# Kernel optimization log

Hardware: AMD Instinct MI355X
Metric: run time of the kernel (lower is better)

## Reference

```python
import jax, jax.numpy as jnp
import numpy as np

B, S, C, H = 2, 512, 25, 768


def setup_inputs() -> dict:
    key = jax.random.key(0)
    ks = jax.random.split(key, 10)
    sc = 1.0 / np.sqrt(H)
    return {
        "token_rep": jax.random.normal(ks[0], (B, S, H), jnp.float32),
        "label_rep": jax.random.normal(ks[1], (B, C, H), jnp.float32),
        # proj_token: Linear(H, 2H) stored as [in, out] for x @ W
        "Wt": jax.random.normal(ks[2], (H, 2 * H), jnp.float32) * sc,
        "bt": jnp.zeros((2 * H,), jnp.float32),
        # proj_label: Linear(H, 2H)
        "Wl": jax.random.normal(ks[3], (H, 2 * H), jnp.float32) * sc,
        "bl": jnp.zeros((2 * H,), jnp.float32),
        # out_mlp[0]: Linear(3H, 4H)
        "W1": jax.random.normal(ks[4], (3 * H, 4 * H), jnp.float32) * (1.0 / np.sqrt(3 * H)),
        "b1": jnp.zeros((4 * H,), jnp.float32),
        # out_mlp[3]: Linear(4H, 3)
        "W2": jax.random.normal(ks[5], (4 * H, 3), jnp.float32) * (1.0 / np.sqrt(4 * H)),
        "b2": jnp.zeros((3,), jnp.float32),
    }


def reference(token_rep, label_rep, Wt, bt, Wl, bl, W1, b1, W2, b2):
    h = token_rep.shape[-1]
    # project and split into (additive half, multiplicative half)
    tp = token_rep @ Wt + bt            # [B,S,2H]
    lp = label_rep @ Wl + bl            # [B,C,2H]
    ta, tb = tp[..., :h], tp[..., h:]
    la, lb = lp[..., :h], lp[..., h:]
    # First MLP layer on concat([ta, la, tb*lb]) without materializing the concat:
    # split W1 row-wise into the three input blocks.
    W1t, W1l, W1p = W1[:h], W1[h:2 * h], W1[2 * h:]
    hid = (ta @ W1t)[:, :, None, :] \
        + (la @ W1l)[:, None, :, :] \
        + jnp.einsum('bsh,bch,hf->bscf', tb, lb, W1p) \
        + b1                            # [B,S,C,4H]
    # Dropout is identity in eval mode.
    return jax.nn.relu(hid) @ W2 + b2   # [B,S,C,3]
```

## Files before the change

kernel.cpp:

```cpp
#include <hip/hip_runtime.h>
#include <hip/hip_bf16.h>
#include <cstdint>
#include <cstddef>

#define BB 2
#define SS 512
#define CC 25
#define HH 768
#define H2 1536
#define H3 2304
#define H4 3072
#define XC_STRIDE ((size_t)96 * 512 * 8)

typedef __attribute__((ext_vector_type(8))) short bf16x8;
typedef __attribute__((ext_vector_type(4))) float f32x4;

#define DEVINL static __device__ __forceinline__

DEVINL unsigned short f2bf(float f) {
  union { float f; unsigned u; } v; v.f = f;
  unsigned r = v.u + 0x7FFF + ((v.u >> 16) & 1);
  return (unsigned short)(r >> 16);
}
DEVINL float bf2f(unsigned short b) {
  union { unsigned u; float f; } v; v.u = ((unsigned)b) << 16; return v.f;
}

DEVINL void async16(const void* g, void* l) {
  __builtin_amdgcn_global_load_lds(
      (const __attribute__((address_space(1))) void*)g,
      (__attribute__((address_space(3))) void*)l, 16, 0, 0);
}

__global__ void k_prep(const float* __restrict__ token,
                       const float* __restrict__ label,
                       const float* __restrict__ b2,
                       const float* __restrict__ Wt,
                       const float* __restrict__ Wl,
                       const float* __restrict__ W1,
                       unsigned short* __restrict__ TC,
                       unsigned short* __restrict__ LC,
                       float* __restrict__ out,
                       unsigned short* __restrict__ WtC,
                       unsigned short* __restrict__ WlC,
                       unsigned short* __restrict__ W1C) {
  __shared__ float tile[64][33];
  const int bid = blockIdx.x;
  const int tid = threadIdx.x;
  if (bid < 408) {
    const float* in;
    unsigned short* o;
    int R, RP, kt, rt;
    if (bid < 384) {
      in = token; o = TC; R = 1024; RP = 1024; kt = bid % 24; rt = bid / 24;
    } else {
      in = label; o = LC; R = 50; RP = 64; kt = bid - 384; rt = 0;
    }
    const int k0 = kt * 32, r0 = rt * 64;
    const int tx = tid & 31, ty = tid >> 5;
#pragma unroll
    for (int i = 0; i < 8; i++) {
      int r = r0 + ty + i * 8;
      tile[ty + i * 8][tx] = in[(size_t)min(r, R - 1) * HH + k0 + tx];
    }
    __syncthreads();
    const int rl = tid & 63, kcl = tid >> 6;
    bf16x8 ov;
#pragma unroll
    for (int j = 0; j < 8; j++) ov[j] = (short)f2bf(tile[rl][kcl * 8 + j]);
    *(bf16x8*)&o[((size_t)((k0 >> 3) + kcl) * RP + r0 + rl) * 8] = ov;
  } else if (bid < 708) {
    int i = (bid - 408) * 256 + tid;
    if (i < BB * SS * CC * 3) out[i] = b2[i % 3];
  } else {
    const int wb = bid - 708;
    const float* in;
    unsigned short* o;
    int N, bx, by;
    if (wb < 3456) {
      in = W1; o = W1C; N = H4; bx = wb % 48; by = wb / 48;
    } else if (wb < 4032) {
      int b = wb - 3456; in = Wt; o = WtC; N = H2; bx = b % 24; by = b / 24;
    } else {
      int b = wb - 4032; in = Wl; o = WlC; N = H2; bx = b % 24; by = b / 24;
    }
    const int f = bx * 64 + (tid & 63);
    const int hc = by * 4 + (tid >> 6);
    bf16x8 ov;
#pragma unroll
    for (int j = 0; j < 8; j++)
      ov[j] = (short)f2bf(in[(size_t)(hc * 8 + j) * N + f]);
    *(bf16x8*)&o[((size_t)hc * N + f) * 8] = ov;
  }
}

DEVINL void mm_kloop(const unsigned short* __restrict__ Ab, int NRA, int MA,
                     int m0, const unsigned short* __restrict__ Bt, int NRB,
                     int n0, unsigned short* As, unsigned short* Bs,
                     f32x4 (&acc)[4][4]) {
  const int tid = threadIdx.x;
  const int lane = tid & 63;
  const int wave = tid >> 6;
  const int q = lane >> 4;
  const int li = lane & 15;
  const int wm = (wave >> 1) * 64;
  const int wn = (wave & 1) * 64;

  int sr[4], skc[4], sra[4];
#pragma unroll
  for (int j = 0; j < 4; j++) {
    int slot = j * 256 + tid;
    skc[j] = slot >> 7;
    sr[j] = slot & 127;
    sra[j] = min(m0 + sr[j], MA - 1);
  }
  auto stage = [&](int kciter) {
#pragma unroll
    for (int j = 0; j < 4; j++) {
      int slot = j * 256 + tid;
      async16(Ab + ((size_t)(kciter + skc[j]) * NRA + sra[j]) * 8,
              (char*)As + slot * 16);
      async16(Bt + ((size_t)(kciter + skc[j]) * NRB + n0 + sr[j]) * 8,
              (char*)Bs + slot * 16);
    }
  };

  stage(0);
  for (int it = 0; it < 12; it++) {
    __syncthreads();
#pragma unroll
    for (int ks = 0; ks < 2; ks++) {
      bf16x8 af[4], bb[4];
#pragma unroll
      for (int mi = 0; mi < 4; mi++)
        af[mi] = *(const bf16x8*)&As[((ks * 4 + q) * 128 + wm + mi * 16 + li) * 8];
#pragma unroll
      for (int ni = 0; ni < 4; ni++)
        bb[ni] = *(const bf16x8*)&Bs[((ks * 4 + q) * 128 + wn + ni * 16 + li) * 8];
#pragma unroll
      for (int mi = 0; mi < 4; mi++)
#pragma unroll
        for (int ni = 0; ni < 4; ni++)
          acc[mi][ni] = __builtin_amdgcn_mfma_f32_16x16x32_bf16(
              af[mi], bb[ni], acc[mi][ni], 0, 0, 0);
    }
    __syncthreads();
    if (it + 1 < 12) stage((it + 1) * 8);
  }
}

__global__ __launch_bounds__(256, 4) void k_mm1(
    const unsigned short* __restrict__ TC, const unsigned short* __restrict__ LC,
    const unsigned short* __restrict__ WtC, const unsigned short* __restrict__ WlC,
    const float* __restrict__ bt, const float* __restrict__ bl,
    unsigned short* __restrict__ TP, unsigned short* __restrict__ LP) {
  __shared__ __align__(16) unsigned short As[8 * 128 * 8];
  __shared__ __align__(16) unsigned short Bs[8 * 128 * 8];
  const int bid = blockIdx.x;
  const int nt = bid % 12, my = bid / 12;
  const bool tok = my < 8;
  const unsigned short* A = tok ? TC : LC;
  const unsigned short* Bt = tok ? WtC : WlC;
  const float* bias = tok ? bt : bl;
  unsigned short* C = tok ? TP : LP;
  const int NRA = tok ? 1024 : 64, MA = tok ? 1024 : 50;
  const int m0 = tok ? my * 128 : 0;
  const int ldc = NRA;
  const int n0 = nt * 128;

  f32x4 acc[4][4];
#pragma unroll
  for (int i = 0; i < 4; i++)
#pragma unroll
    for (int j = 0; j < 4; j++) acc[i][j] = (f32x4){0.f, 0.f, 0.f, 0.f};
  mm_kloop(A, NRA, MA, m0, Bt, H2, n0, As, Bs, acc);

  const int lane = threadIdx.x & 63, wave = threadIdx.x >> 6;
  const int q = lane >> 4, li = lane & 15;
  const int wm = (wave >> 1) * 64, wn = (wave & 1) * 64;
#pragma unroll
  for (int mi = 0; mi < 4; mi++)
#pragma unroll
    for (int rr = 0; rr < 4; rr++) {
      int row = m0 + wm + mi * 16 + q * 4 + rr;
      if (row < MA) {
#pragma unroll
        for (int ni = 0; ni < 4; ni++) {
          int col = n0 + wn + ni * 16 + li;
          C[((size_t)(col >> 3) * ldc + row) * 8 + (col & 7)] =
              f2bf(acc[mi][ni][rr] + bias[col]);
        }
      }
    }
}

__global__ __launch_bounds__(256, 4) void k_mm2(
    const unsigned short* __restrict__ TP, const unsigned short* __restrict__ LP,
    const unsigned short* __restrict__ W1C,
    float* __restrict__ base, float* __restrict__ al,
    unsigned short* __restrict__ XC) {
  __shared__ __align__(16) unsigned short As[8 * 128 * 8];
  __shared__ __align__(16) unsigned short Bs[8 * 128 * 8];
  const int bid = blockIdx.x;
  if (bid < 216) {
    const int nt = bid % 24, my = bid / 24;
    const bool tok = my < 8;
    const unsigned short* A = tok ? TP : LP;
    const unsigned short* Bt = tok ? W1C : W1C + (size_t)96 * H4 * 8;
    float* Cf = tok ? base : al;
    const int NRA = tok ? 1024 : 64, MA = tok ? 1024 : 50;
    const int m0 = tok ? my * 128 : 0;
    const int n0 = nt * 128;

    f32x4 acc[4][4];
#pragma unroll
    for (int i = 0; i < 4; i++)
#pragma unroll
      for (int j = 0; j < 4; j++) acc[i][j] = (f32x4){0.f, 0.f, 0.f, 0.f};
    mm_kloop(A, NRA, MA, m0, Bt, H4, n0, As, Bs, acc);

    const int lane = threadIdx.x & 63, wave = threadIdx.x >> 6;
    const int q = lane >> 4, li = lane & 15;
    const int wm = (wave >> 1) * 64, wn = (wave & 1) * 64;
#pragma unroll
    for (int mi = 0; mi < 4; mi++)
#pragma unroll
      for (int rr = 0; rr < 4; rr++) {
        int row = m0 + wm + mi * 16 + q * 4 + rr;
        if (row < MA) {
#pragma unroll
          for (int ni = 0; ni < 4; ni++) {
            int col = n0 + wn + ni * 16 + li;
            Cf[(size_t)row * H4 + col] = acc[mi][ni][rr];
          }
        }
      }
  } else {
    const int i = bid - 216;
    const int bc = i / 192;
    const int rem = i % 192;
    const int hc = rem >> 1;
    const int s = (rem & 1) * 256 + threadIdx.x;
    const int b = bc / CC;
    bf16x8 tv = *(const bf16x8*)&TP[((size_t)(96 + hc) * 1024 + b * 512 + s) * 8];
    bf16x8 lv = *(const bf16x8*)&LP[((size_t)(96 + hc) * 64 + bc) * 8];
    bf16x8 o;
#pragma unroll
    for (int j = 0; j < 8; j++)
      o[j] = (short)f2bf(bf2f((unsigned short)tv[j]) * bf2f((unsigned short)lv[j]));
    *(bf16x8*)&XC[(size_t)bc * XC_STRIDE + ((size_t)hc * 512 + s) * 8] = o;
  }
}

__global__ __launch_bounds__(256, 4) void k_scorer(
    const unsigned short* __restrict__ XC,
    const unsigned short* __restrict__ Bt,
    const float* __restrict__ base, const float* __restrict__ al,
    const float* __restrict__ b1, const float* __restrict__ W2,
    float* __restrict__ out) {
  __shared__ __align__(16) unsigned short As[8 * 128 * 8];
  __shared__ __align__(16) unsigned short Bs[8 * 128 * 8];
  const int tid = threadIdx.x;
  const int lane = tid & 63;
  const int wave = tid >> 6;
  const int q = lane >> 4;
  const int li = lane & 15;
  const int wm = (wave >> 1) * 64;
  const int wn = (wave & 1) * 64;

  const int n0 = blockIdx.x * 128;
  const int bc = blockIdx.y >> 2;
  const int m0 = (blockIdx.y & 3) * 128;
  const unsigned short* Ab = XC + (size_t)bc * XC_STRIDE;

  f32x4 acc[4][4];
#pragma unroll
  for (int i = 0; i < 4; i++)
#pragma unroll
    for (int j = 0; j < 4; j++) acc[i][j] = (f32x4){0.f, 0.f, 0.f, 0.f};
  mm_kloop(Ab, 512, 512, m0, Bt, H4, n0, As, Bs, acc);

  const int b = bc / CC, c = bc % CC;
  int fcol[4];
  float alb[4];
#pragma unroll
  for (int ni = 0; ni < 4; ni++) {
    int f = n0 + wn + ni * 16 + li;
    fcol[ni] = f;
    alb[ni] = al[(size_t)bc * H4 + f] + b1[f];
  }
  bf16x8 w2f[2];
#pragma unroll
  for (int ks = 0; ks < 2; ks++)
#pragma unroll
    for (int jj = 0; jj < 8; jj++) {
      int f = n0 + wn + ks * 32 + q * 8 + jj;
      float v = (li < 3) ? W2[(size_t)f * 3 + li] : 0.f;
      w2f[ks][jj] = (short)f2bf(v);
    }
  unsigned short* Ew = (unsigned short*)((char*)As + wave * 2304);

#pragma unroll
  for (int mi = 0; mi < 4; mi++) {
    float bs[4][4];
#pragma unroll
    for (int rr = 0; rr < 4; rr++) {
      int s_l = m0 + wm + mi * 16 + q * 4 + rr;
      const float* bp = base + (size_t)(b * SS + s_l) * H4;
#pragma unroll
      for (int ni = 0; ni < 4; ni++) bs[ni][rr] = bp[fcol[ni]];
    }
#pragma unroll
    for (int rr = 0; rr < 4; rr++)
#pragma unroll
      for (int ni = 0; ni < 4; ni++) {
        float v = acc[mi][ni][rr] + bs[ni][rr] + alb[ni];
        v = fmaxf(v, 0.f);
        Ew[(q * 4 + rr) * 72 + ni * 16 + li] = f2bf(v);
      }
    f32x4 oc = (f32x4){0.f, 0.f, 0.f, 0.f};
#pragma unroll
    for (int ks = 0; ks < 2; ks++) {
      bf16x8 ef = *(const bf16x8*)&Ew[li * 72 + ks * 32 + q * 8];
      oc = __builtin_amdgcn_mfma_f32_16x16x32_bf16(ef, w2f[ks], oc, 0, 0, 0);
    }
#pragma unroll
    for (int rr = 0; rr < 4; rr++) {
      int s_l = m0 + wm + mi * 16 + q * 4 + rr;
      if (li < 3)
        atomicAdd(&out[((size_t)(b * SS + s_l) * CC + c) * 3 + li], oc[rr]);
    }
  }
}


extern "C" void kernel_launch(void* const* d_in, const int* in_sizes, int n_in,
                              void* d_out, int out_size, void* d_ws, size_t ws_size,
                              hipStream_t stream) {
  (void)in_sizes; (void)n_in; (void)ws_size; (void)out_size;
  const float* token = (const float*)d_in[0];
  const float* label = (const float*)d_in[1];
  const float* Wt    = (const float*)d_in[2];
  const float* bt    = (const float*)d_in[3];
  const float* Wl    = (const float*)d_in[4];
  const float* bl    = (const float*)d_in[5];
  const float* W1    = (const float*)d_in[6];
  const float* b1    = (const float*)d_in[7];
  const float* W2    = (const float*)d_in[8];
  const float* b2    = (const float*)d_in[9];
  float* out = (float*)d_out;

  char* p = (char*)d_ws;
  auto alloc = [&](size_t bytes) {
    char* r = p;
    p += (bytes + 255) & ~(size_t)255;
    return r;
  };
  unsigned short* TC  = (unsigned short*)alloc((size_t)96 * 1024 * 8 * 2);
  unsigned short* LC  = (unsigned short*)alloc((size_t)96 * 64 * 8 * 2);
  unsigned short* WtC = (unsigned short*)alloc((size_t)96 * 1536 * 8 * 2);
  unsigned short* WlC = (unsigned short*)alloc((size_t)96 * 1536 * 8 * 2);
  unsigned short* W1C = (unsigned short*)alloc((size_t)288 * 3072 * 8 * 2);
  unsigned short* TP  = (unsigned short*)alloc((size_t)192 * 1024 * 8 * 2);
  unsigned short* LP  = (unsigned short*)alloc((size_t)192 * 64 * 8 * 2);
  unsigned short* XC  = (unsigned short*)alloc((size_t)CC * BB * XC_STRIDE * 2);
  float* base = (float*)alloc((size_t)BB * SS * H4 * 4);
  float* al   = (float*)alloc((size_t)BB * CC * H4 * 4);

  k_prep<<<5316, 256, 0, stream>>>(token, label, b2, Wt, Wl, W1,
                                   TC, LC, out, WtC, WlC, W1C);
  k_mm1<<<108, 256, 0, stream>>>(TC, LC, WtC, WlC, bt, bl, TP, LP);
  k_mm2<<<9816, 256, 0, stream>>>(TP, LP, W1C, base, al, XC);
  k_scorer<<<dim3(24, 200), 256, 0, stream>>>(
      XC, W1C + (size_t)192 * H4 * 8, base, al, b1, W2, out);
}
```

Before: 273.9 us.

## Double-buffer GEMM k-loop staging and store base/label partials in bf16

The shared GEMM k-loop moves from a single 8-chunk shared tile with two barriers per iteration to a two-buffer ping-pong of 4-chunk tiles with one barrier. The next tile's async loads are issued before the current tile's MFMAs, so global loads can overlap compute. Separately, the token and label partial products of the first MLP layer are stored as bf16, with b1 folded into the label part, instead of fp32. This halves their write and read traffic in the scorer epilogue, at the cost of an extra rounding step, and an added barrier protects reuse of shared memory in the epilogue.

```diff
diff --git a/kernel.cpp b/kernel.cpp
--- a/kernel.cpp
+++ b/kernel.cpp
@@ -106,46 +106,44 @@
   const int wm = (wave >> 1) * 64;
   const int wn = (wave & 1) * 64;
 
-  int sr[4], skc[4], sra[4];
-#pragma unroll
-  for (int j = 0; j < 4; j++) {
+  int sr[2], skc[2], sra[2];
+#pragma unroll
+  for (int j = 0; j < 2; j++) {
     int slot = j * 256 + tid;
     skc[j] = slot >> 7;
     sr[j] = slot & 127;
     sra[j] = min(m0 + sr[j], MA - 1);
   }
-  auto stage = [&](int kciter) {
-#pragma unroll
-    for (int j = 0; j < 4; j++) {
+  auto stage = [&](int kcbase, int buf) {
+#pragma unroll
+    for (int j = 0; j < 2; j++) {
       int slot = j * 256 + tid;
-      async16(Ab + ((size_t)(kciter + skc[j]) * NRA + sra[j]) * 8,
-              (char*)As + slot * 16);
-      async16(Bt + ((size_t)(kciter + skc[j]) * NRB + n0 + sr[j]) * 8,
-              (char*)Bs + slot * 16);
+      async16(Ab + ((size_t)(kcbase + skc[j]) * NRA + sra[j]) * 8,
+              (char*)As + buf * 8192 + slot * 16);
+      async16(Bt + ((size_t)(kcbase + skc[j]) * NRB + n0 + sr[j]) * 8,
+              (char*)Bs + buf * 8192 + slot * 16);
     }
   };
 
-  stage(0);
-  for (int it = 0; it < 12; it++) {
+  stage(0, 0);
+  for (int it = 0; it < 24; it++) {
     __syncthreads();
-#pragma unroll
-    for (int ks = 0; ks < 2; ks++) {
-      bf16x8 af[4], bb[4];
-#pragma unroll
-      for (int mi = 0; mi < 4; mi++)
-        af[mi] = *(const bf16x8*)&As[((ks * 4 + q) * 128 + wm + mi * 16 + li) * 8];
+    if (it + 1 < 24) stage((it + 1) * 4, (it + 1) & 1);
+    const unsigned short* Ac = As + (it & 1) * 4096;
+    const unsigned short* Bc = Bs + (it & 1) * 4096;
+    bf16x8 af[4], bb[4];
+#pragma unroll
+    for (int mi = 0; mi < 4; mi++)
+      af[mi] = *(const bf16x8*)&Ac[(q * 128 + wm + mi * 16 + li) * 8];
+#pragma unroll
+    for (int ni = 0; ni < 4; ni++)
+      bb[ni] = *(const bf16x8*)&Bc[(q * 128 + wn + ni * 16 + li) * 8];
+#pragma unroll
+    for (int mi = 0; mi < 4; mi++)
 #pragma unroll
       for (int ni = 0; ni < 4; ni++)
-        bb[ni] = *(const bf16x8*)&Bs[((ks * 4 + q) * 128 + wn + ni * 16 + li) * 8];
-#pragma unroll
-      for (int mi = 0; mi < 4; mi++)
-#pragma unroll
-        for (int ni = 0; ni < 4; ni++)
-          acc[mi][ni] = __builtin_amdgcn_mfma_f32_16x16x32_bf16(
-              af[mi], bb[ni], acc[mi][ni], 0, 0, 0);
-    }
-    __syncthreads();
-    if (it + 1 < 12) stage((it + 1) * 8);
+        acc[mi][ni] = __builtin_amdgcn_mfma_f32_16x16x32_bf16(
+            af[mi], bb[ni], acc[mi][ni], 0, 0, 0);
   }
 }
 
@@ -154,8 +152,8 @@
     const unsigned short* __restrict__ WtC, const unsigned short* __restrict__ WlC,
     const float* __restrict__ bt, const float* __restrict__ bl,
     unsigned short* __restrict__ TP, unsigned short* __restrict__ LP) {
-  __shared__ __align__(16) unsigned short As[8 * 128 * 8];
-  __shared__ __align__(16) unsigned short Bs[8 * 128 * 8];
+  __shared__ __align__(16) unsigned short As[2 * 4096];
+  __shared__ __align__(16) unsigned short Bs[2 * 4096];
   const int bid = blockIdx.x;
   const int nt = bid % 12, my = bid / 12;
   const bool tok = my < 8;
@@ -196,18 +194,18 @@
 
 __global__ __launch_bounds__(256, 4) void k_mm2(
     const unsigned short* __restrict__ TP, const unsigned short* __restrict__ LP,
-    const unsigned short* __restrict__ W1C,
-    float* __restrict__ base, float* __restrict__ al,
+    const unsigned short* __restrict__ W1C, const float* __restrict__ b1,
+    unsigned short* __restrict__ bbase, unsigned short* __restrict__ albf,
     unsigned short* __restrict__ XC) {
-  __shared__ __align__(16) unsigned short As[8 * 128 * 8];
-  __shared__ __align__(16) unsigned short Bs[8 * 128 * 8];
+  __shared__ __align__(16) unsigned short As[2 * 4096];
+  __shared__ __align__(16) unsigned short Bs[2 * 4096];
   const int bid = blockIdx.x;
   if (bid < 216) {
     const int nt = bid % 24, my = bid / 24;
     const bool tok = my < 8;
     const unsigned short* A = tok ? TP : LP;
     const unsigned short* Bt = tok ? W1C : W1C + (size_t)96 * H4 * 8;
-    float* Cf = tok ? base : al;
+    unsigned short* Cb = tok ? bbase : albf;
     const int NRA = tok ? 1024 : 64, MA = tok ? 1024 : 50;
     const int m0 = tok ? my * 128 : 0;
     const int n0 = nt * 128;
@@ -231,7 +229,8 @@
 #pragma unroll
           for (int ni = 0; ni < 4; ni++) {
             int col = n0 + wn + ni * 16 + li;
-            Cf[(size_t)row * H4 + col] = acc[mi][ni][rr];
+            float v = acc[mi][ni][rr] + (tok ? 0.f : b1[col]);
+            Cb[(size_t)row * H4 + col] = f2bf(v);
           }
         }
       }
@@ -255,11 +254,12 @@
 __global__ __launch_bounds__(256, 4) void k_scorer(
     const unsigned short* __restrict__ XC,
     const unsigned short* __restrict__ Bt,
-    const float* __restrict__ base, const float* __restrict__ al,
-    const float* __restrict__ b1, const float* __restrict__ W2,
+    const unsigned short* __restrict__ bbase,
+    const unsigned short* __restrict__ albf,
+    const float* __restrict__ W2,
     float* __restrict__ out) {
-  __shared__ __align__(16) unsigned short As[8 * 128 * 8];
-  __shared__ __align__(16) unsigned short Bs[8 * 128 * 8];
+  __shared__ __align__(16) unsigned short As[2 * 4096];
+  __shared__ __align__(16) unsigned short Bs[2 * 4096];
   const int tid = threadIdx.x;
   const int lane = tid & 63;
   const int wave = tid >> 6;
@@ -280,6 +280,8 @@
     for (int j = 0; j < 4; j++) acc[i][j] = (f32x4){0.f, 0.f, 0.f, 0.f};
   mm_kloop(Ab, 512, 512, m0, Bt, H4, n0, As, Bs, acc);
 
+  __syncthreads();
+
   const int b = bc / CC, c = bc % CC;
   int fcol[4];
   float alb[4];
@@ -287,7 +289,7 @@
   for (int ni = 0; ni < 4; ni++) {
     int f = n0 + wn + ni * 16 + li;
     fcol[ni] = f;
-    alb[ni] = al[(size_t)bc * H4 + f] + b1[f];
+    alb[ni] = bf2f(albf[(size_t)bc * H4 + f]);
   }
   bf16x8 w2f[2];
 #pragma unroll
@@ -306,9 +308,9 @@
 #pragma unroll
     for (int rr = 0; rr < 4; rr++) {
       int s_l = m0 + wm + mi * 16 + q * 4 + rr;
-      const float* bp = base + (size_t)(b * SS + s_l) * H4;
-#pragma unroll
-      for (int ni = 0; ni < 4; ni++) bs[ni][rr] = bp[fcol[ni]];
+      const unsigned short* bp = bbase + (size_t)(b * SS + s_l) * H4;
+#pragma unroll
+      for (int ni = 0; ni < 4; ni++) bs[ni][rr] = bf2f(bp[fcol[ni]]);
     }
 #pragma unroll
     for (int rr = 0; rr < 4; rr++)
@@ -364,13 +366,13 @@
   unsigned short* TP  = (unsigned short*)alloc((size_t)192 * 1024 * 8 * 2);
   unsigned short* LP  = (unsigned short*)alloc((size_t)192 * 64 * 8 * 2);
   unsigned short* XC  = (unsigned short*)alloc((size_t)CC * BB * XC_STRIDE * 2);
-  float* base = (float*)alloc((size_t)BB * SS * H4 * 4);
-  float* al   = (float*)alloc((size_t)BB * CC * H4 * 4);
+  unsigned short* bbase = (unsigned short*)alloc((size_t)BB * SS * H4 * 2);
+  unsigned short* albf  = (unsigned short*)alloc((size_t)BB * CC * H4 * 2);
 
   k_prep<<<5316, 256, 0, stream>>>(token, label, b2, Wt, Wl, W1,
                                    TC, LC, out, WtC, WlC, W1C);
   k_mm1<<<108, 256, 0, stream>>>(TC, LC, WtC, WlC, bt, bl, TP, LP);
-  k_mm2<<<9816, 256, 0, stream>>>(TP, LP, W1C, base, al, XC);
+  k_mm2<<<9816, 256, 0, stream>>>(TP, LP, W1C, b1, bbase, albf, XC);
   k_scorer<<<dim3(24, 200), 256, 0, stream>>>(
-      XC, W1C + (size_t)192 * H4 * 8, base, al, b1, W2, out);
-}
+      XC, W1C + (size_t)192 * H4 * 8, bbase, albf, W2, out);
+}
```

After: 296.1 us. +8.1%, slower.

## Enlarge scorer M-tile to 256 and store base/label partials in bf16

Applied to the files above, without the earlier changes.

The scorer kernel now computes a 256x128 tile per block: each wave holds 8x4 MFMA accumulators, loads a double-sized A tile in its own inlined k-loop, and the grid is halved. This reuses every B (W1p) tile across twice as many rows, cutting global and LDS traffic per FLOP. Separately, the token and label first-layer partials are written as bf16 with b1 folded into the label term, halving the epilogue's reads of base. The costs are more registers (launch bounds lowered to 3 waves per SIMD), less occupancy, a non-double-buffered loop, and extra rounding of the partial sums.

```diff
diff --git a/kernel.cpp b/kernel.cpp
--- a/kernel.cpp
+++ b/kernel.cpp
@@ -196,8 +196,8 @@
 
 __global__ __launch_bounds__(256, 4) void k_mm2(
     const unsigned short* __restrict__ TP, const unsigned short* __restrict__ LP,
-    const unsigned short* __restrict__ W1C,
-    float* __restrict__ base, float* __restrict__ al,
+    const unsigned short* __restrict__ W1C, const float* __restrict__ b1,
+    unsigned short* __restrict__ bbase, unsigned short* __restrict__ albf,
     unsigned short* __restrict__ XC) {
   __shared__ __align__(16) unsigned short As[8 * 128 * 8];
   __shared__ __align__(16) unsigned short Bs[8 * 128 * 8];
@@ -207,7 +207,7 @@
     const bool tok = my < 8;
     const unsigned short* A = tok ? TP : LP;
     const unsigned short* Bt = tok ? W1C : W1C + (size_t)96 * H4 * 8;
-    float* Cf = tok ? base : al;
+    unsigned short* Cb = tok ? bbase : albf;
     const int NRA = tok ? 1024 : 64, MA = tok ? 1024 : 50;
     const int m0 = tok ? my * 128 : 0;
     const int n0 = nt * 128;
@@ -231,7 +231,8 @@
 #pragma unroll
           for (int ni = 0; ni < 4; ni++) {
             int col = n0 + wn + ni * 16 + li;
-            Cf[(size_t)row * H4 + col] = acc[mi][ni][rr];
+            float v = acc[mi][ni][rr] + (tok ? 0.f : b1[col]);
+            Cb[(size_t)row * H4 + col] = f2bf(v);
           }
         }
       }
@@ -252,33 +253,72 @@
   }
 }
 
-__global__ __launch_bounds__(256, 4) void k_scorer(
+__global__ __launch_bounds__(256, 3) void k_scorer(
     const unsigned short* __restrict__ XC,
     const unsigned short* __restrict__ Bt,
-    const float* __restrict__ base, const float* __restrict__ al,
-    const float* __restrict__ b1, const float* __restrict__ W2,
+    const unsigned short* __restrict__ bbase,
+    const unsigned short* __restrict__ albf,
+    const float* __restrict__ W2,
     float* __restrict__ out) {
-  __shared__ __align__(16) unsigned short As[8 * 128 * 8];
+  __shared__ __align__(16) unsigned short As[8 * 256 * 8];
   __shared__ __align__(16) unsigned short Bs[8 * 128 * 8];
   const int tid = threadIdx.x;
   const int lane = tid & 63;
   const int wave = tid >> 6;
   const int q = lane >> 4;
   const int li = lane & 15;
-  const int wm = (wave >> 1) * 64;
+  const int wm = (wave >> 1) * 128;
   const int wn = (wave & 1) * 64;
 
   const int n0 = blockIdx.x * 128;
-  const int bc = blockIdx.y >> 2;
-  const int m0 = (blockIdx.y & 3) * 128;
+  const int bc = blockIdx.y >> 1;
+  const int m0 = (blockIdx.y & 1) * 256;
   const unsigned short* Ab = XC + (size_t)bc * XC_STRIDE;
 
-  f32x4 acc[4][4];
-#pragma unroll
-  for (int i = 0; i < 4; i++)
+  f32x4 acc[8][4];
+#pragma unroll
+  for (int i = 0; i < 8; i++)
 #pragma unroll
     for (int j = 0; j < 4; j++) acc[i][j] = (f32x4){0.f, 0.f, 0.f, 0.f};
-  mm_kloop(Ab, 512, 512, m0, Bt, H4, n0, As, Bs, acc);
+
+  auto stage = [&](int kcbase) {
+#pragma unroll
+    for (int j = 0; j < 8; j++) {
+      int slot = j * 256 + tid;
+      async16(Ab + ((size_t)(kcbase + (slot >> 8)) * 512 + m0 + (slot & 255)) * 8,
+              (char*)As + slot * 16);
+    }
+#pragma unroll
+    for (int j = 0; j < 4; j++) {
+      int slot = j * 256 + tid;
+      async16(Bt + ((size_t)(kcbase + (slot >> 7)) * H4 + n0 + (slot & 127)) * 8,
+              (char*)Bs + slot * 16);
+    }
+  };
+
+  stage(0);
+  for (int it = 0; it < 12; it++) {
+    __syncthreads();
+#pragma unroll
+    for (int ks = 0; ks < 2; ks++) {
+      bf16x8 bb[4];
+#pragma unroll
+      for (int ni = 0; ni < 4; ni++)
+        bb[ni] = *(const bf16x8*)&Bs[((ks * 4 + q) * 128 + wn + ni * 16 + li) * 8];
+#pragma unroll
+      for (int mi = 0; mi < 8; mi++) {
+        bf16x8 af = *(const bf16x8*)&As[((ks * 4 + q) * 256 + wm + mi * 16 + li) * 8];
+#pragma unroll
+        for (int ni = 0; ni < 4; ni++)
+          acc[mi][ni] = __builtin_amdgcn_mfma_f32_16x16x32_bf16(
+              af, bb[ni], acc[mi][ni], 0, 0, 0);
+      }
+    }
+    __syncthreads();
+    if (it + 1 < 12) stage((it + 1) * 8);
+  }
+
+  __syncthreads();
 
   const int b = bc / CC, c = bc % CC;
   int fcol[4];
@@ -287,7 +327,7 @@
   for (int ni = 0; ni < 4; ni++) {
     int f = n0 + wn + ni * 16 + li;
     fcol[ni] = f;
-    alb[ni] = al[(size_t)bc * H4 + f] + b1[f];
+    alb[ni] = bf2f(albf[(size_t)bc * H4 + f]);
   }
   bf16x8 w2f[2];
 #pragma unroll
@@ -301,14 +341,14 @@
   unsigned short* Ew = (unsigned short*)((char*)As + wave * 2304);
 
 #pragma unroll
-  for (int mi = 0; mi < 4; mi++) {
+  for (int mi = 0; mi < 8; mi++) {
     float bs[4][4];
 #pragma unroll
     for (int rr = 0; rr < 4; rr++) {
       int s_l = m0 + wm + mi * 16 + q * 4 + rr;
-      const float* bp = base + (size_t)(b * SS + s_l) * H4;
-#pragma unroll
-      for (int ni = 0; ni < 4; ni++) bs[ni][rr] = bp[fcol[ni]];
+      const unsigned short* bp = bbase + (size_t)(b * SS + s_l) * H4;
+#pragma unroll
+      for (int ni = 0; ni < 4; ni++) bs[ni][rr] = bf2f(bp[fcol[ni]]);
     }
 #pragma unroll
     for (int rr = 0; rr < 4; rr++)
@@ -364,13 +404,13 @@
   unsigned short* TP  = (unsigned short*)alloc((size_t)192 * 1024 * 8 * 2);
   unsigned short* LP  = (unsigned short*)alloc((size_t)192 * 64 * 8 * 2);
   unsigned short* XC  = (unsigned short*)alloc((size_t)CC * BB * XC_STRIDE * 2);
-  float* base = (float*)alloc((size_t)BB * SS * H4 * 4);
-  float* al   = (float*)alloc((size_t)BB * CC * H4 * 4);
+  unsigned short* bbase = (unsigned short*)alloc((size_t)BB * SS * H4 * 2);
+  unsigned short* albf  = (unsigned short*)alloc((size_t)BB * CC * H4 * 2);
 
   k_prep<<<5316, 256, 0, stream>>>(token, label, b2, Wt, Wl, W1,
                                    TC, LC, out, WtC, WlC, W1C);
   k_mm1<<<108, 256, 0, stream>>>(TC, LC, WtC, WlC, bt, bl, TP, LP);
-  k_mm2<<<9816, 256, 0, stream>>>(TP, LP, W1C, base, al, XC);
-  k_scorer<<<dim3(24, 200), 256, 0, stream>>>(
-      XC, W1C + (size_t)192 * H4 * 8, base, al, b1, W2, out);
-}
+  k_mm2<<<9816, 256, 0, stream>>>(TP, LP, W1C, b1, bbase, albf, XC);
+  k_scorer<<<dim3(24, 100), 256, 0, stream>>>(
+      XC, W1C + (size_t)192 * H4 * 8, bbase, albf, W2, out);
+}
```

Result: slower. 392.0 us (+43.1%).
